# Optimization experiments

Hardware: AMD Instinct MI355X
Metric: run time of the kernel (lower is better)

Reference implementation:

```python
import jax, jax.numpy as jnp
import numpy as np

DIM = 128      # encoder output dim
D_OUT = 10     # num classes
T = 1.0        # temperature
EPS = 1e-7


def setup_inputs() -> dict:
    key = jax.random.key(0)
    ks = jax.random.split(key, 5)
    B, N, D_IN = 512, 100000, 128
    x = jax.random.normal(ks[0], (B, D_IN), jnp.float32)
    candidate_x = jax.random.normal(ks[1], (N, D_IN), jnp.float32)
    candidate_y = jax.random.randint(ks[2], (N,), 0, D_OUT, dtype=jnp.int32)
    W = jax.random.normal(ks[3], (DIM, D_IN), jnp.float32) / np.sqrt(D_IN).astype(np.float32)
    b = jax.random.normal(ks[4], (DIM,), jnp.float32) * 0.01
    return {"x": x, "candidate_x": candidate_x, "candidate_y": candidate_y, "W": W, "b": b}


def reference(x, candidate_x, candidate_y, W, b):
    # Linear encoder (n_blocks == 0 path)
    h = x @ W.T + b              # [B, DIM]
    hc = candidate_x @ W.T + b   # [N, DIM]
    # Pairwise L2 distances via the Gram expansion (same math as torch.cdist p=2)
    d2 = (jnp.sum(h * h, axis=-1, keepdims=True)
          + jnp.sum(hc * hc, axis=-1)[None, :]
          - 2.0 * (h @ hc.T))    # [B, N]
    dist = jnp.sqrt(jnp.maximum(d2, 0.0)) / T
    # Attention-like masked softmax over candidates (eval: no diagonal mask)
    p = jax.nn.softmax(-dist, axis=-1)              # [B, N]
    onehot_y = jax.nn.one_hot(candidate_y, D_OUT, dtype=p.dtype)  # [N, D_OUT]
    logits = p @ onehot_y                           # [B, D_OUT]
    return jnp.log(logits + EPS)
```

## Files before the change

kernel.cpp:

```cpp
#include <hip/hip_runtime.h>
#include <stdint.h>

typedef __bf16 bf16x8 __attribute__((ext_vector_type(8)));
typedef float f32x4 __attribute__((ext_vector_type(4)));
typedef short short8 __attribute__((ext_vector_type(8)));
typedef unsigned int uint2v __attribute__((ext_vector_type(2)));
typedef float float4_t __attribute__((ext_vector_type(4)));

#define LOG2E 1.44269504088896340736f

union FragU { short8 s; bf16x8 b; };
union YbU { uint2v u2[2]; bf16x8 b; };

#define DEVI static __device__ __forceinline__

DEVI f32x4 mfma16(bf16x8 a, bf16x8 b, f32x4 c) {
  return __builtin_amdgcn_mfma_f32_16x16x32_bf16(a, b, c, 0, 0, 0);
}

DEVI bf16x8 cvt8(float4_t a, float4_t b) {
  bf16x8 r;
  r[0] = (__bf16)a[0]; r[1] = (__bf16)a[1]; r[2] = (__bf16)a[2]; r[3] = (__bf16)a[3];
  r[4] = (__bf16)b[0]; r[5] = (__bf16)b[1]; r[6] = (__bf16)b[2]; r[7] = (__bf16)b[3];
  return r;
}

__global__ __launch_bounds__(256, 3) void prep_encode_kernel(
    const float* __restrict__ cx, const float* __restrict__ x,
    const float* __restrict__ W, const float* __restrict__ bias,
    const int* __restrict__ y,
    unsigned short* __restrict__ HC, float* __restrict__ hcn,
    unsigned short* __restrict__ Hm, float* __restrict__ hnm,
    unsigned short* __restrict__ YT,
    int N, int Bm, int NP, int NBA, int NBB, int bpc) {
  __shared__ __align__(16) unsigned short Wl[128 * 128];

  const int bid = blockIdx.x, t = threadIdx.x;
  const int NB_ENC = NBA + NBB;

  if (bid >= NB_ENC) {
    if (bid == NB_ENC) {
      int i = N + t;
      if (i < NP) hcn[i] = 1e30f;
    } else {
      int k = bid - NB_ENC - 1;
      int c = k / bpc, j = k - c * bpc;
      int n0 = j * 2048 + t * 8;
      unsigned short* dst = YT + (size_t)c * NP + n0;
#pragma unroll
      for (int e = 0; e < 8; ++e) {
        int n = n0 + e;
        if (n < NP) dst[e] = (n < N && y[n] == c) ? 0x3F80u : 0u;
      }
    }
    return;
  }

  const float* in;
  unsigned short* outh;
  float* outnorm;
  int M, blk;
  if (bid < NBA) {
    in = cx; outh = HC; outnorm = hcn; M = N; blk = bid;
  } else {
    in = x; outh = Hm; outnorm = hnm; M = Bm; blk = bid - NBA;
  }

  const int lane = t & 63, w = t >> 6;
  const int g = lane >> 4, q = lane & 15;
  const int rowbase = blk * 64 + w * 16;

  float4_t iv[8];
  const int arow = rowbase + q;
  const bool av = arow < M;
  {
    int ar = av ? arow : 0;
    const float* src = in + (size_t)ar * 128 + g * 8;
#pragma unroll
    for (int kc = 0; kc < 4; ++kc) {
      iv[2 * kc] = *(const float4_t*)(src + kc * 32);
      iv[2 * kc + 1] = *(const float4_t*)(src + kc * 32 + 4);
    }
  }

  {
    int row = t >> 1, half = t & 1;
    const float* wsrc = W + row * 128 + half * 64;
    float4_t wv[16];
#pragma unroll
    for (int j = 0; j < 16; ++j) wv[j] = *(const float4_t*)(wsrc + j * 4);
#pragma unroll
    for (int j = 0; j < 8; ++j) {
      FragU u; u.b = cvt8(wv[2 * j], wv[2 * j + 1]);
      int slot = (half * 8 + j) ^ (row & 7);
      *(short8*)((char*)Wl + row * 256 + slot * 16) = u.s;
    }
  }
  __syncthreads();

  bf16x8 a[4];
#pragma unroll
  for (int kc = 0; kc < 4; ++kc) {
    FragU u; u.b = cvt8(iv[2 * kc], iv[2 * kc + 1]);
    if (!av) u.s = short8{0, 0, 0, 0, 0, 0, 0, 0};
    a[kc] = u.b;
  }

  f32x4 acc[8];
#pragma unroll
  for (int nt = 0; nt < 8; ++nt) acc[nt] = f32x4{0.f, 0.f, 0.f, 0.f};
#pragma unroll
  for (int nt = 0; nt < 8; ++nt) {
    int brow = nt * 16 + q;
#pragma unroll
    for (int kc = 0; kc < 4; ++kc) {
      int slot = (kc * 4 + g) ^ (brow & 7);
      FragU u;
      u.s = *(const short8*)((const char*)Wl + brow * 256 + slot * 16);
      acc[nt] = mfma16(a[kc], u.b, acc[nt]);
    }
  }

  float nsq[4] = {0.f, 0.f, 0.f, 0.f};
#pragma unroll
  for (int nt = 0; nt < 8; ++nt) {
    int col = nt * 16 + q;
    float bv = bias[col];
#pragma unroll
    for (int r = 0; r < 4; ++r) {
      int row = rowbase + g * 4 + r;
      float val = (acc[nt][r] + bv) * LOG2E;
      __bf16 h = (__bf16)val;
      float vf = (float)h;
      nsq[r] += vf * vf;
      union { __bf16 h; unsigned short u; } cv; cv.h = h;
      if (row < M) outh[(size_t)row * 128 + col] = cv.u;
    }
  }
#pragma unroll
  for (int m = 1; m < 16; m <<= 1) {
#pragma unroll
    for (int r = 0; r < 4; ++r) nsq[r] += __shfl_xor(nsq[r], m, 64);
  }
  if (q == 0) {
#pragma unroll
    for (int r = 0; r < 4; ++r) {
      int row = rowbase + g * 4 + r;
      if (row < M) outnorm[row] = nsq[r];
    }
  }
}

__global__ __launch_bounds__(512, 4) void nca_main(
    const unsigned short* __restrict__ H, const float* __restrict__ hnorm,
    const unsigned short* __restrict__ HC, const float* __restrict__ hcnorm,
    const unsigned short* __restrict__ YT, float* __restrict__ part,
    int B, int N, int NP, int NT, int CHUNKS) {
  __shared__ __align__(16) unsigned short HCl[2][64 * 128];

  const int t = threadIdx.x, lane = t & 63, w = t >> 6;
  const int g = lane >> 4, q = lane & 15;
  const int rg = blockIdx.y, chunk = blockIdx.x;
  const int t0 = (int)(((long long)chunk * NT) / CHUNKS);
  const int t1 = (int)(((long long)(chunk + 1) * NT) / CHUNKS);

  bf16x8 hfrag[2][4];
  float hn[2];
  int hrow[2];
#pragma unroll
  for (int s = 0; s < 2; ++s) {
    hrow[s] = rg * 256 + s * 128 + w * 16 + q;
    bool v = hrow[s] < B;
    int ar = v ? hrow[s] : 0;
#pragma unroll
    for (int kc = 0; kc < 4; ++kc) {
      FragU u;
      u.s = *(const short8*)(H + (size_t)ar * 128 + kc * 32 + g * 8);
      if (!v) u.s = short8{0, 0, 0, 0, 0, 0, 0, 0};
      hfrag[s][kc] = u.b;
    }
    hn[s] = hnorm[ar];
  }

  int soff[4];
#pragma unroll
  for (int kc = 0; kc < 4; ++kc)
    soff[kc] = q * 256 + (((kc * 4 + g) ^ (q & 7)) << 4);

  const int srow = t >> 4;
  const int sslot = (t & 15) ^ (srow & 7);
  const int g_off = srow * 256 + sslot * 16;
  const int l_off = w * 1024;
  const char* HCc = (const char*)HC;

  f32x4 pool0 = f32x4{0.f, 0.f, 0.f, 0.f};
  f32x4 pool1 = f32x4{0.f, 0.f, 0.f, 0.f};

#define STAGE(TT, BUF)                                                         \
  {                                                                            \
    const char* src = HCc + (size_t)(TT)*16384 + g_off;                        \
    char* lb = (char*)HCl[BUF] + l_off;                                        \
    __builtin_amdgcn_global_load_lds(                                          \
        (const __attribute__((address_space(1))) unsigned int*)src,            \
        (__attribute__((address_space(3))) unsigned int*)lb, 16, 0, 0);        \
    __builtin_amdgcn_global_load_lds(                                          \
        (const __attribute__((address_space(1))) unsigned int*)(src + 8192),   \
        (__attribute__((address_space(3))) unsigned int*)(lb + 8192), 16, 0,   \
        0);                                                                    \
  }

  int cur = 0;
  if (t0 < t1) STAGE(t0, 0);

  for (int tt = t0; tt < t1; ++tt) {
    __syncthreads();
    if (tt + 1 < t1) STAGE(tt + 1, cur ^ 1);

    const int colbase = tt * 64;
    float4_t cnv[4];
    uint2v ytu[4];
#pragma unroll
    for (int ns = 0; ns < 4; ++ns) {
      cnv[ns] = *(const float4_t*)(hcnorm + colbase + ns * 16 + g * 4);
      ytu[ns] = *(const uint2v*)(YT + (size_t)q * NP + colbase + ns * 16 + g * 4);
    }

    const char* lb = (const char*)HCl[cur];
    f32x4 a0[4], a1[4];
#pragma unroll
    for (int ns = 0; ns < 4; ++ns) {
      a0[ns] = f32x4{0.f, 0.f, 0.f, 0.f};
      a1[ns] = f32x4{0.f, 0.f, 0.f, 0.f};
    }
#pragma unroll
    for (int ns = 0; ns < 4; ++ns) {
#pragma unroll
      for (int kc = 0; kc < 4; ++kc) {
        FragU u;
        u.s = *(const short8*)(lb + soff[kc] + ns * 4096);
        a0[ns] = mfma16(u.b, hfrag[0][kc], a0[ns]);
        a1[ns] = mfma16(u.b, hfrag[1][kc], a1[ns]);
      }
    }

#pragma unroll
    for (int ns = 0; ns < 4; ++ns) {
      FragU wb0, wb1;
      wb0.s = short8{0, 0, 0, 0, 0, 0, 0, 0};
      wb1.s = short8{0, 0, 0, 0, 0, 0, 0, 0};
#pragma unroll
      for (int r = 0; r < 4; ++r) {
        float c0 = hn[0] + cnv[ns][r];
        float c1 = hn[1] + cnv[ns][r];
        float d20 = fmaxf(fmaf(-2.f, a0[ns][r], c0), 0.f);
        float d21 = fmaxf(fmaf(-2.f, a1[ns][r], c1), 0.f);
        float di0 = __builtin_amdgcn_sqrtf(d20);
        float di1 = __builtin_amdgcn_sqrtf(d21);
        wb0.b[r] = (__bf16)__builtin_amdgcn_exp2f(-di0);
        wb1.b[r] = (__bf16)__builtin_amdgcn_exp2f(-di1);
      }
      YbU yb;
      yb.u2[0] = ytu[ns];
      yb.u2[1] = uint2v{0u, 0u};
      pool0 = mfma16(yb.b, wb0.b, pool0);
      pool1 = mfma16(yb.b, wb1.b, pool1);
    }
    cur ^= 1;
  }
#undef STAGE

  if (hrow[0] < B)
    *(f32x4*)(part + ((size_t)hrow[0] * CHUNKS + chunk) * 16 + g * 4) = pool0;
  if (hrow[1] < B)
    *(f32x4*)(part + ((size_t)hrow[1] * CHUNKS + chunk) * 16 + g * 4) = pool1;
}

__global__ __launch_bounds__(256) void finalize_kernel(
    const float* __restrict__ part, float* __restrict__ out, int B,
    int CHUNKS) {
  const int w = threadIdx.x >> 6, t = threadIdx.x & 63;
  const int row = blockIdx.x * 4 + w;
  if (row >= B) return;
  const int c = t & 15, grp = t >> 4;
  const float* p = part + (size_t)row * CHUNKS * 16;
  float s = 0.f;
  for (int j = grp; j < CHUNKS; j += 4) s += p[j * 16 + c];
  s += __shfl_xor(s, 16, 64);
  s += __shfl_xor(s, 32, 64);
  float Z = 0.f;
#pragma unroll
  for (int cc = 0; cc < 10; ++cc) Z += __shfl(s, cc, 64);
  if (t < 10) out[row * 10 + t] = logf(fmaf(s, 1.f / Z, 1e-7f));
}

extern "C" void kernel_launch(void* const* d_in, const int* in_sizes, int n_in,
                              void* d_out, int out_size, void* d_ws,
                              size_t ws_size, hipStream_t stream) {
  const float* x = (const float*)d_in[0];
  const float* cx = (const float*)d_in[1];
  const int* cy = (const int*)d_in[2];
  const float* W = (const float*)d_in[3];
  const float* b = (const float*)d_in[4];
  const int B = in_sizes[0] / 128;
  const int N = in_sizes[1] / 128;
  float* out = (float*)d_out;

  const int NT = (N + 63) / 64;
  const int NP = NT * 64;
  const int RG = (B + 255) / 256;

  char* ws = (char*)d_ws;
  size_t o = 0;
  auto alloc = [&](size_t bytes) {
    size_t r = o;
    o += (bytes + 255) & ~(size_t)255;
    return r;
  };
  unsigned short* HC = (unsigned short*)(ws + alloc((size_t)N * 128 * 2));
  float* hcn = (float*)(ws + alloc((size_t)NP * 4 + 16384));
  unsigned short* H = (unsigned short*)(ws + alloc((size_t)B * 128 * 2));
  float* hn = (float*)(ws + alloc((size_t)B * 4));
  unsigned short* YT = (unsigned short*)(ws + alloc((size_t)16 * NP * 2));

  size_t avail = (ws_size > o) ? (ws_size - o) : 0;
  int CHUNKS = (int)(avail / ((size_t)B * 16 * 4));
  if (CHUNKS > 256) CHUNKS = 256;
  if (CHUNKS < 32) CHUNKS = 32;
  float* part = (float*)(ws + alloc((size_t)CHUNKS * B * 16 * 4));

  const int NBA = (N + 63) / 64, NBB = (B + 63) / 64;
  const int bpc = (NP + 2047) / 2048;
  prep_encode_kernel<<<NBA + NBB + 1 + 16 * bpc, 256, 0, stream>>>(
      cx, x, W, b, cy, HC, hcn, H, hn, YT, N, B, NP, NBA, NBB, bpc);

  dim3 grid(CHUNKS, RG);
  nca_main<<<grid, 512, 0, stream>>>(H, hn, HC, hcn, YT, part, B, N, NP, NT,
                                     CHUNKS);
  finalize_kernel<<<(B + 3) / 4, 256, 0, stream>>>(part, out, B, CHUNKS);
}
```

Before: 162.3 us.

## Triple-buffer candidate tiles with vmcnt waits and double rows per encode block

```diff
diff --git a/kernel.cpp b/kernel.cpp
--- a/kernel.cpp
+++ b/kernel.cpp
@@ -68,18 +68,21 @@
 
   const int lane = t & 63, w = t >> 6;
   const int g = lane >> 4, q = lane & 15;
-  const int rowbase = blk * 64 + w * 16;
-
-  float4_t iv[8];
-  const int arow = rowbase + q;
-  const bool av = arow < M;
-  {
-    int ar = av ? arow : 0;
+  const int rb = blk * 128 + w * 16;
+
+  float4_t iv[2][8];
+  int arow[2];
+  bool av[2];
+#pragma unroll
+  for (int s = 0; s < 2; ++s) {
+    arow[s] = rb + s * 64 + q;
+    av[s] = arow[s] < M;
+    int ar = av[s] ? arow[s] : 0;
     const float* src = in + (size_t)ar * 128 + g * 8;
 #pragma unroll
     for (int kc = 0; kc < 4; ++kc) {
-      iv[2 * kc] = *(const float4_t*)(src + kc * 32);
-      iv[2 * kc + 1] = *(const float4_t*)(src + kc * 32 + 4);
+      iv[s][2 * kc] = *(const float4_t*)(src + kc * 32);
+      iv[s][2 * kc + 1] = *(const float4_t*)(src + kc * 32 + 4);
     }
   }
 
@@ -98,17 +101,21 @@
   }
   __syncthreads();
 
-  bf16x8 a[4];
-#pragma unroll
-  for (int kc = 0; kc < 4; ++kc) {
-    FragU u; u.b = cvt8(iv[2 * kc], iv[2 * kc + 1]);
-    if (!av) u.s = short8{0, 0, 0, 0, 0, 0, 0, 0};
-    a[kc] = u.b;
-  }
-
-  f32x4 acc[8];
-#pragma unroll
-  for (int nt = 0; nt < 8; ++nt) acc[nt] = f32x4{0.f, 0.f, 0.f, 0.f};
+  bf16x8 a[2][4];
+#pragma unroll
+  for (int s = 0; s < 2; ++s)
+#pragma unroll
+    for (int kc = 0; kc < 4; ++kc) {
+      FragU u; u.b = cvt8(iv[s][2 * kc], iv[s][2 * kc + 1]);
+      if (!av[s]) u.s = short8{0, 0, 0, 0, 0, 0, 0, 0};
+      a[s][kc] = u.b;
+    }
+
+  f32x4 acc[2][8];
+#pragma unroll
+  for (int s = 0; s < 2; ++s)
+#pragma unroll
+    for (int nt = 0; nt < 8; ++nt) acc[s][nt] = f32x4{0.f, 0.f, 0.f, 0.f};
 #pragma unroll
   for (int nt = 0; nt < 8; ++nt) {
     int brow = nt * 16 + q;
@@ -117,37 +124,45 @@
       int slot = (kc * 4 + g) ^ (brow & 7);
       FragU u;
       u.s = *(const short8*)((const char*)Wl + brow * 256 + slot * 16);
-      acc[nt] = mfma16(a[kc], u.b, acc[nt]);
-    }
-  }
-
-  float nsq[4] = {0.f, 0.f, 0.f, 0.f};
+      acc[0][nt] = mfma16(a[0][kc], u.b, acc[0][nt]);
+      acc[1][nt] = mfma16(a[1][kc], u.b, acc[1][nt]);
+    }
+  }
+
+  float nsq[2][4] = {{0.f, 0.f, 0.f, 0.f}, {0.f, 0.f, 0.f, 0.f}};
 #pragma unroll
   for (int nt = 0; nt < 8; ++nt) {
     int col = nt * 16 + q;
     float bv = bias[col];
 #pragma unroll
-    for (int r = 0; r < 4; ++r) {
-      int row = rowbase + g * 4 + r;
-      float val = (acc[nt][r] + bv) * LOG2E;
-      __bf16 h = (__bf16)val;
-      float vf = (float)h;
-      nsq[r] += vf * vf;
-      union { __bf16 h; unsigned short u; } cv; cv.h = h;
-      if (row < M) outh[(size_t)row * 128 + col] = cv.u;
+    for (int s = 0; s < 2; ++s) {
+#pragma unroll
+      for (int r = 0; r < 4; ++r) {
+        int row = rb + s * 64 + g * 4 + r;
+        float val = (acc[s][nt][r] + bv) * LOG2E;
+        __bf16 h = (__bf16)val;
+        float vf = (float)h;
+        nsq[s][r] += vf * vf;
+        union { __bf16 h; unsigned short u; } cv; cv.h = h;
+        if (row < M) outh[(size_t)row * 128 + col] = cv.u;
+      }
     }
   }
 #pragma unroll
   for (int m = 1; m < 16; m <<= 1) {
 #pragma unroll
-    for (int r = 0; r < 4; ++r) nsq[r] += __shfl_xor(nsq[r], m, 64);
+    for (int s = 0; s < 2; ++s)
+#pragma unroll
+      for (int r = 0; r < 4; ++r) nsq[s][r] += __shfl_xor(nsq[s][r], m, 64);
   }
   if (q == 0) {
 #pragma unroll
-    for (int r = 0; r < 4; ++r) {
-      int row = rowbase + g * 4 + r;
-      if (row < M) outnorm[row] = nsq[r];
-    }
+    for (int s = 0; s < 2; ++s)
+#pragma unroll
+      for (int r = 0; r < 4; ++r) {
+        int row = rb + s * 64 + g * 4 + r;
+        if (row < M) outnorm[row] = nsq[s][r];
+      }
   }
 }
 
@@ -156,7 +171,7 @@
     const unsigned short* __restrict__ HC, const float* __restrict__ hcnorm,
     const unsigned short* __restrict__ YT, float* __restrict__ part,
     int B, int N, int NP, int NT, int CHUNKS) {
-  __shared__ __align__(16) unsigned short HCl[2][64 * 128];
+  __shared__ __align__(16) unsigned short HCl[3 * 64 * 128];
 
   const int t = threadIdx.x, lane = t & 63, w = t >> 6;
   const int g = lane >> 4, q = lane & 15;
@@ -196,25 +211,31 @@
   f32x4 pool0 = f32x4{0.f, 0.f, 0.f, 0.f};
   f32x4 pool1 = f32x4{0.f, 0.f, 0.f, 0.f};
 
-#define STAGE(TT, BUF)                                                         \
+#define STAGE(TT, BI)                                                          \
   {                                                                            \
-    const char* src = HCc + (size_t)(TT)*16384 + g_off;                        \
-    char* lb = (char*)HCl[BUF] + l_off;                                        \
+    const char* src_ = HCc + (size_t)(TT)*16384 + g_off;                       \
+    char* lb_ = (char*)HCl + (BI)*16384 + l_off;                               \
     __builtin_amdgcn_global_load_lds(                                          \
-        (const __attribute__((address_space(1))) unsigned int*)src,            \
-        (__attribute__((address_space(3))) unsigned int*)lb, 16, 0, 0);        \
+        (const __attribute__((address_space(1))) unsigned int*)src_,           \
+        (__attribute__((address_space(3))) unsigned int*)lb_, 16, 0, 0);       \
     __builtin_amdgcn_global_load_lds(                                          \
-        (const __attribute__((address_space(1))) unsigned int*)(src + 8192),   \
-        (__attribute__((address_space(3))) unsigned int*)(lb + 8192), 16, 0,   \
+        (const __attribute__((address_space(1))) unsigned int*)(src_ + 8192),  \
+        (__attribute__((address_space(3))) unsigned int*)(lb_ + 8192), 16, 0,  \
         0);                                                                    \
   }
 
-  int cur = 0;
   if (t0 < t1) STAGE(t0, 0);
-
+  if (t0 + 1 < t1) STAGE(t0 + 1, 1);
+
+  int bi = 0;
   for (int tt = t0; tt < t1; ++tt) {
-    __syncthreads();
-    if (tt + 1 < t1) STAGE(tt + 1, cur ^ 1);
+    if (tt + 1 < t1) {
+      asm volatile("s_waitcnt vmcnt(2)" ::: "memory");
+    } else {
+      asm volatile("s_waitcnt vmcnt(0)" ::: "memory");
+    }
+    __builtin_amdgcn_s_barrier();
+    __builtin_amdgcn_sched_barrier(0);
 
     const int colbase = tt * 64;
     float4_t cnv[4];
@@ -224,48 +245,56 @@
       cnv[ns] = *(const float4_t*)(hcnorm + colbase + ns * 16 + g * 4);
       ytu[ns] = *(const uint2v*)(YT + (size_t)q * NP + colbase + ns * 16 + g * 4);
     }
-
-    const char* lb = (const char*)HCl[cur];
-    f32x4 a0[4], a1[4];
-#pragma unroll
-    for (int ns = 0; ns < 4; ++ns) {
-      a0[ns] = f32x4{0.f, 0.f, 0.f, 0.f};
-      a1[ns] = f32x4{0.f, 0.f, 0.f, 0.f};
-    }
-#pragma unroll
-    for (int ns = 0; ns < 4; ++ns) {
-#pragma unroll
-      for (int kc = 0; kc < 4; ++kc) {
-        FragU u;
-        u.s = *(const short8*)(lb + soff[kc] + ns * 4096);
-        a0[ns] = mfma16(u.b, hfrag[0][kc], a0[ns]);
-        a1[ns] = mfma16(u.b, hfrag[1][kc], a1[ns]);
-      }
-    }
-
-#pragma unroll
-    for (int ns = 0; ns < 4; ++ns) {
-      FragU wb0, wb1;
-      wb0.s = short8{0, 0, 0, 0, 0, 0, 0, 0};
-      wb1.s = short8{0, 0, 0, 0, 0, 0, 0, 0};
-#pragma unroll
-      for (int r = 0; r < 4; ++r) {
-        float c0 = hn[0] + cnv[ns][r];
-        float c1 = hn[1] + cnv[ns][r];
-        float d20 = fmaxf(fmaf(-2.f, a0[ns][r], c0), 0.f);
-        float d21 = fmaxf(fmaf(-2.f, a1[ns][r], c1), 0.f);
-        float di0 = __builtin_amdgcn_sqrtf(d20);
-        float di1 = __builtin_amdgcn_sqrtf(d21);
-        wb0.b[r] = (__bf16)__builtin_amdgcn_exp2f(-di0);
-        wb1.b[r] = (__bf16)__builtin_amdgcn_exp2f(-di1);
-      }
-      YbU yb;
-      yb.u2[0] = ytu[ns];
-      yb.u2[1] = uint2v{0u, 0u};
-      pool0 = mfma16(yb.b, wb0.b, pool0);
-      pool1 = mfma16(yb.b, wb1.b, pool1);
-    }
-    cur ^= 1;
+    __builtin_amdgcn_sched_barrier(0);
+
+    int bs = bi + 2; if (bs >= 3) bs -= 3;
+    if (tt + 2 < t1) STAGE(tt + 2, bs);
+
+    const char* lb = (const char*)HCl + bi * 16384;
+#pragma unroll
+    for (int nsg = 0; nsg < 2; ++nsg) {
+      f32x4 a0[2], a1[2];
+#pragma unroll
+      for (int k = 0; k < 2; ++k) {
+        a0[k] = f32x4{0.f, 0.f, 0.f, 0.f};
+        a1[k] = f32x4{0.f, 0.f, 0.f, 0.f};
+      }
+#pragma unroll
+      for (int k = 0; k < 2; ++k) {
+        int ns = nsg * 2 + k;
+#pragma unroll
+        for (int kc = 0; kc < 4; ++kc) {
+          FragU u;
+          u.s = *(const short8*)(lb + soff[kc] + ns * 4096);
+          a0[k] = mfma16(u.b, hfrag[0][kc], a0[k]);
+          a1[k] = mfma16(u.b, hfrag[1][kc], a1[k]);
+        }
+      }
+#pragma unroll
+      for (int k = 0; k < 2; ++k) {
+        int ns = nsg * 2 + k;
+        FragU wb0, wb1;
+        wb0.s = short8{0, 0, 0, 0, 0, 0, 0, 0};
+        wb1.s = short8{0, 0, 0, 0, 0, 0, 0, 0};
+#pragma unroll
+        for (int r = 0; r < 4; ++r) {
+          float c0 = hn[0] + cnv[ns][r];
+          float c1 = hn[1] + cnv[ns][r];
+          float d20 = fmaxf(fmaf(-2.f, a0[k][r], c0), 0.f);
+          float d21 = fmaxf(fmaf(-2.f, a1[k][r], c1), 0.f);
+          float di0 = __builtin_amdgcn_sqrtf(d20);
+          float di1 = __builtin_amdgcn_sqrtf(d21);
+          wb0.b[r] = (__bf16)__builtin_amdgcn_exp2f(-di0);
+          wb1.b[r] = (__bf16)__builtin_amdgcn_exp2f(-di1);
+        }
+        YbU yb;
+        yb.u2[0] = ytu[ns];
+        yb.u2[1] = uint2v{0u, 0u};
+        pool0 = mfma16(yb.b, wb0.b, pool0);
+        pool1 = mfma16(yb.b, wb1.b, pool1);
+      }
+    }
+    ++bi; if (bi == 3) bi = 0;
   }
 #undef STAGE
 
@@ -328,7 +357,7 @@
   if (CHUNKS < 32) CHUNKS = 32;
   float* part = (float*)(ws + alloc((size_t)CHUNKS * B * 16 * 4));
 
-  const int NBA = (N + 63) / 64, NBB = (B + 63) / 64;
+  const int NBA = (N + 127) / 128, NBB = (B + 127) / 128;
   const int bpc = (NP + 2047) / 2048;
   prep_encode_kernel<<<NBA + NBB + 1 + 16 * bpc, 256, 0, stream>>>(
       cx, x, W, b, cy, HC, hcn, H, hn, YT, N, B, NP, NBA, NBB, bpc);
```

Result: no change. 161.3 us (-0.6%).
